# Kernel optimization log

Measured on AMD Instinct MI355X. Metric: run time of the kernel, lower is better.

## Reference

```python
import jax, jax.numpy as jnp
import numpy as np

N = 100000   # nodes
E = 800000   # edges
H = 128      # hidden_dim
HOP = 3
B = 64       # graphs


def setup_inputs() -> dict:
    key = jax.random.key(0)
    ks = jax.random.split(key, 24)
    s = 0.05
    x = jnp.round(jax.random.uniform(ks[0], (N, 1))).astype(jnp.float32)  # binary node indicator
    edge_index = jax.random.randint(ks[1], (2, E), 0, N)
    edge_attr = jax.random.normal(ks[2], (E, 1), dtype=jnp.float32)
    batch = jnp.sort(jax.random.randint(ks[3], (N,), 0, B))
    p = lambda k, sh: (s * jax.random.normal(k, sh)).astype(jnp.float32)
    return dict(
        x=x, edge_index=edge_index, edge_attr=edge_attr, batch=batch, num_graphs=B,
        l0_w=p(ks[4], (HOP, 1, H)), l0_b=p(ks[5], (HOP, H)),
        l1_w=p(ks[6], (HOP, H, H)), l1_b=p(ks[7], (HOP, H)),
        l2_w=p(ks[8], (HOP, 1, H)), l2_b=p(ks[9], (HOP, H)),
        l3_w=p(ks[10], (HOP, 1, 1)), l3_b=p(ks[11], (HOP, 1)),
        att_w=p(ks[12], (2 * H, H)), att_b=p(ks[13], (H,)),
        sp_w=p(ks[14], (H, H)), sp_b=p(ks[15], (H,)),
        ac_w=p(ks[16], (2 * H, H)), ac_b=p(ks[17], (H,)),
        last_w=p(ks[18], (2 * H, 1)), last_b=p(ks[19], (1,)),
    )


def _seg_mean(v, idx, m):
    # scatter-mean into m buckets; empty buckets -> 0 (matches PyG MeanAggregation)
    s = jax.ops.segment_sum(v, idx, num_segments=m)
    c = jax.ops.segment_sum(jnp.ones((v.shape[0], 1), v.dtype), idx, num_segments=m)
    return jnp.where(c > 0, s / jnp.maximum(c, 1.0), 0.0)


def reference(x, edge_index, edge_attr, batch, num_graphs,
              l0_w, l0_b, l1_w, l1_b, l2_w, l2_b, l3_w, l3_b,
              att_w, att_b, sp_w, sp_b, ac_w, ac_b, last_w, last_b):
    n = x.shape[0]
    row, col = edge_index[0], edge_index[1]
    hop, hid = l0_w.shape[0], l0_w.shape[2]
    u = jnp.zeros((n, hid), x.dtype)
    for i in range(hop):
        first = x @ l0_w[i] + l0_b[i]                      # [N,H]
        u_agg = _seg_mean(edge_attr * u[col], row, n)      # gather + scatter-mean
        second = u_agg @ l1_w[i] + l1_b[i]
        ee = jax.nn.relu(edge_attr @ l3_w[i] + l3_b[i])    # [E,1]
        third = _seg_mean(ee, row, n) @ l2_w[i] + l2_b[i]
        u = jax.nn.relu(first + second + third)
    # per-graph cluster embeddings (global_mean_pool ratios)
    h_c_0 = _seg_mean(u * (1 - x), batch, num_graphs) / _seg_mean(1 - x, batch, num_graphs)
    h_c_1 = _seg_mean(u * x, batch, num_graphs) / _seg_mean(x, batch, num_graphs)
    hc0, hc1 = h_c_0[batch], h_c_1[batch]                  # [N,H]
    tce = x * hc0 + (1 - x) * hc1
    h_a = jnp.concatenate([u, tce], axis=-1)               # [N,2H]
    att = h_a @ att_w + att_b
    w0 = jnp.sum(att * hc0, axis=1, keepdims=True)
    w1 = jnp.sum(att * hc1, axis=1, keepdims=True)
    w = jax.nn.softmax(jnp.concatenate([w0, w1], axis=-1), axis=-1)
    h_s = w[:, :1] * hc0 + w[:, 1:] * hc1
    q = jnp.concatenate([h_s @ sp_w + sp_b, h_a @ ac_w + ac_b], axis=-1) @ last_w + last_b
    return q
```

## Files before the change

### kernel.cpp

```cpp
#include <hip/hip_runtime.h>
#include <stdint.h>

typedef unsigned int  u32;
typedef unsigned short u16;

typedef short bf16x8 __attribute__((ext_vector_type(8)));
typedef float f32x4  __attribute__((ext_vector_type(4)));

static __device__ __forceinline__ float b2f(u16 h){
    union { u32 u; float f; } v; v.u = ((u32)h) << 16; return v.f;
}
static __device__ __forceinline__ float b2f_hi(u32 w){
    union { u32 u; float f; } v; v.u = w & 0xFFFF0000u; return v.f;
}
static __device__ __forceinline__ float b2f_lo(u32 w){
    union { u32 u; float f; } v; v.u = w << 16; return v.f;
}
static __device__ __forceinline__ u16 f2b(float f){
    union { float f; u32 u; } v; v.f = f;
    u32 r = v.u + 0x7FFFu + ((v.u >> 16) & 1u);
    return (u16)(r >> 16);
}

#define OL0W 0
#define OL0B 384
#define OL1W 768
#define OL1B 49920
#define OL2W 50304
#define OL2B 50688
#define OL3W 51072
#define OL3B 51075
#define OATTW 51078
#define OATTB 83846
#define OSPW 83974
#define OSPB 100358
#define OACW 100486
#define OACB 133254
#define OLASTW 133382
#define OLASTB 133638
#define WTOT 133639

#define PREPW_BLOCKS 192
#define ECAP 40

struct Ptrs16 { const void* p[16]; };

static __device__ __forceinline__ int detect_bf(const u32* __restrict__ xw){
    int lane = threadIdx.x & 63;
    int f = 0;
    #pragma unroll
    for (int i = 0; i < 8; ++i){
        u32 w = xw[lane * 8 + i];
        f |= ((w & 0xFFFFu) == 0x3F80u) ? 1 : 0;
    }
    return __ballot(f) != 0ull;
}

__global__ __launch_bounds__(256) void k_prep(Ptrs16 wp, const void* __restrict__ xin,
                                              float* __restrict__ wc, float* __restrict__ xc,
                                              u16* __restrict__ w1t, float* __restrict__ basev,
                                              int* __restrict__ flag,
                                              const int* __restrict__ row, const int* __restrict__ col,
                                              const void* __restrict__ ea,
                                              int* __restrict__ cnt, int2* __restrict__ ecs,
                                              int scatBase, int E, int N){
    int b = blockIdx.x, t = threadIdx.x;
    int bf = detect_bf((const u32*)xin);
    if (b >= scatBase){
        int e0 = ((b - scatBase) * 256 + t) * 4;
        if (e0 >= E) return;
        int rr[4], cc[4]; float av[4];
        if (e0 + 3 < E){
            int4 rv = *(const int4*)(row + e0);
            int4 cv = *(const int4*)(col + e0);
            rr[0]=rv.x; rr[1]=rv.y; rr[2]=rv.z; rr[3]=rv.w;
            cc[0]=cv.x; cc[1]=cv.y; cc[2]=cv.z; cc[3]=cv.w;
            if (bf){
                ushort4 ev = *(const ushort4*)((const u16*)ea + e0);
                av[0]=b2f(ev.x); av[1]=b2f(ev.y); av[2]=b2f(ev.z); av[3]=b2f(ev.w);
            } else {
                float4 ev = *(const float4*)((const float*)ea + e0);
                av[0]=ev.x; av[1]=ev.y; av[2]=ev.z; av[3]=ev.w;
            }
        } else {
            #pragma unroll
            for (int j = 0; j < 4; ++j){
                int e = e0 + j;
                rr[j] = (e < E) ? row[e] : 0;
                cc[j] = (e < E) ? col[e] : 0;
                av[j] = (e < E) ? (bf ? b2f(((const u16*)ea)[e]) : ((const float*)ea)[e]) : 0.f;
            }
        }
        int slot[4];
        #pragma unroll
        for (int j = 0; j < 4; ++j)
            slot[j] = (e0 + j < E) ? atomicAdd(&cnt[rr[j]], 1) : ECAP;
        #pragma unroll
        for (int j = 0; j < 4; ++j)
            if (e0 + j < E && slot[j] < ECAP)
                ecs[(size_t)rr[j] * ECAP + slot[j]] = make_int2(cc[j], __float_as_int(av[j]));
        return;
    }
    auto rd = [&](int seg, int off) -> float {
        return bf ? b2f(((const u16*)wp.p[seg])[off]) : ((const float*)wp.p[seg])[off];
    };
    if (b < PREPW_BLOCKS){
        int id = b * 256 + t;
        int i = id >> 14, rem = id & 16383;
        int n = rem >> 7, k = rem & 127;
        w1t[(i * 128 + n) * 128 + k] = f2b(rd(2, (i * 128 + k) * 128 + n));
        if (id < 384) basev[id] = rd(1, id) + rd(3, id) + rd(5, id);
        if (id == 0) *flag = bf;
    } else {
        int i = (b - PREPW_BLOCKS) * 256 + t;
        const int sz[16] = {384,384,49152,384,384,384,3,3,32768,128,16384,128,32768,128,256,1};
        if (i < WTOT){
            int seg = 0, off = i;
            while (off >= sz[seg]){ off -= sz[seg]; ++seg; }
            wc[i] = rd(seg, off);
        } else {
            int n = i - WTOT;
            if (n < N) xc[n] = bf ? b2f(((const u16*)xin)[n]) : ((const float*)xin)[n];
        }
    }
}

__global__ __launch_bounds__(256) void k_hop0(const int2* __restrict__ ecs, const int* __restrict__ cnt,
                                              const float* __restrict__ xc, const float* __restrict__ wc,
                                              float* __restrict__ t12,
                                              const float* __restrict__ basev, uint4* __restrict__ uOut, int N){
    int id = blockIdx.x * 256 + threadIdx.x;
    int n = id >> 4;
    if (n >= N) return;
    int sl = threadIdx.x & 15;
    float w30 = wc[OL3W + 0], w31 = wc[OL3W + 1], w32 = wc[OL3W + 2];
    float c30 = wc[OL3B + 0], c31 = wc[OL3B + 1], c32 = wc[OL3B + 2];
    int d = min(cnt[n], ECAP);
    size_t s = (size_t)n * ECAP;
    float s0 = 0.f, s1 = 0.f, s2 = 0.f;
    for (int e = sl; e < d; e += 16){
        float a = __int_as_float(ecs[s + e].y);
        s0 += fmaxf(a * w30 + c30, 0.f);
        s1 += fmaxf(a * w31 + c31, 0.f);
        s2 += fmaxf(a * w32 + c32, 0.f);
    }
    #pragma unroll
    for (int m = 1; m < 16; m <<= 1){
        s0 += __shfl_xor(s0, m);
        s1 += __shfl_xor(s1, m);
        s2 += __shfl_xor(s2, m);
    }
    float iv = d > 0 ? 1.0f / (float)d : 0.f;
    if (sl == 0){ t12[n] = s1 * iv; t12[N + n] = s2 * iv; }
    float t0 = s0 * iv;
    float xv = xc[n];
    int j = sl * 8;
    const float* l0wc = wc + OL0W;
    const float* l2wc = wc + OL2W;
    u32 w[4];
    #pragma unroll
    for (int k = 0; k < 4; ++k){
        float va = fmaxf(xv * l0wc[j + 2*k]     + t0 * l2wc[j + 2*k]     + basev[j + 2*k],     0.f);
        float vb = fmaxf(xv * l0wc[j + 2*k + 1] + t0 * l2wc[j + 2*k + 1] + basev[j + 2*k + 1], 0.f);
        w[k] = (u32)f2b(va) | ((u32)f2b(vb) << 16);
    }
    uOut[id] = make_uint4(w[0], w[1], w[2], w[3]);
}

#define ACC8(acc, g, p) \
    acc[0] += g * b2f_lo(p.x); acc[1] += g * b2f_hi(p.x); \
    acc[2] += g * b2f_lo(p.y); acc[3] += g * b2f_hi(p.y); \
    acc[4] += g * b2f_lo(p.z); acc[5] += g * b2f_hi(p.z); \
    acc[6] += g * b2f_lo(p.w); acc[7] += g * b2f_hi(p.w);

__global__ __launch_bounds__(256) void k_hop(const u16* __restrict__ uPrev, u16* __restrict__ uNext,
    const int2* __restrict__ ecs, const int* __restrict__ cnt,
    const u16* __restrict__ w1t, const float* __restrict__ basev,
    const float* __restrict__ l0wc, const float* __restrict__ l2wc,
    const float* __restrict__ xc, const float* __restrict__ t_i, int N)
{
    __shared__ __align__(16) u16 A[32][136];
    int tid = threadIdx.x;
    int lane = tid & 63, wid = tid >> 6;
    int n0 = blockIdx.x * 32;
    int cid = lane & 15, grp = lane >> 4;

    #pragma unroll
    for (int p = 0; p < 2; ++p){
        int r = wid * 8 + p * 4 + grp;
        int n = n0 + r;
        float acc[8];
        #pragma unroll
        for (int j = 0; j < 8; ++j) acc[j] = 0.f;
        if (n < N){
            int d = min(cnt[n], ECAP);
            size_t s = (size_t)n * ECAP;
            for (int e = 0; e < d; e += 8){
                int idx[8]; float g[8]; int2 m[8]; uint4 pv[8];
                idx[0] = e;
                #pragma unroll
                for (int j = 1; j < 8; ++j) idx[j] = (e + j < d) ? e + j : 0;
                #pragma unroll
                for (int j = 0; j < 8; ++j) m[j] = ecs[s + idx[j]];
                g[0] = __int_as_float(m[0].y);
                #pragma unroll
                for (int j = 1; j < 8; ++j) g[j] = (e + j < d) ? __int_as_float(m[j].y) : 0.f;
                #pragma unroll
                for (int j = 0; j < 8; ++j) pv[j] = *(const uint4*)(uPrev + (size_t)m[j].x * 128 + cid * 8);
                #pragma unroll
                for (int j = 0; j < 8; ++j){ ACC8(acc, g[j], pv[j]); }
            }
            float sc = d > 0 ? 1.0f / (float)d : 0.f;
            uint4 o;
            o.x = (u32)f2b(acc[0] * sc) | ((u32)f2b(acc[1] * sc) << 16);
            o.y = (u32)f2b(acc[2] * sc) | ((u32)f2b(acc[3] * sc) << 16);
            o.z = (u32)f2b(acc[4] * sc) | ((u32)f2b(acc[5] * sc) << 16);
            o.w = (u32)f2b(acc[6] * sc) | ((u32)f2b(acc[7] * sc) << 16);
            *(uint4*)&A[r][cid * 8] = o;
        } else {
            *(uint4*)&A[r][cid * 8] = make_uint4(0u, 0u, 0u, 0u);
        }
    }
    __syncthreads();

    bf16x8 bfr[4][2];
    #pragma unroll
    for (int kk = 0; kk < 4; ++kk)
        #pragma unroll
        for (int nt = 0; nt < 2; ++nt)
            bfr[kk][nt] = *(const bf16x8*)(w1t + (size_t)(wid * 32 + nt * 16 + cid) * 128 + kk * 32 + grp * 8);

    f32x4 acc4[2][2];
    #pragma unroll
    for (int mt = 0; mt < 2; ++mt)
        #pragma unroll
        for (int nt = 0; nt < 2; ++nt) acc4[mt][nt] = (f32x4){0.f, 0.f, 0.f, 0.f};
    #pragma unroll
    for (int kk = 0; kk < 4; ++kk){
        int kb = kk * 32 + grp * 8;
        bf16x8 af[2];
        #pragma unroll
        for (int mt = 0; mt < 2; ++mt) af[mt] = *(const bf16x8*)&A[mt * 16 + cid][kb];
        #pragma unroll
        for (int mt = 0; mt < 2; ++mt)
            #pragma unroll
            for (int nt = 0; nt < 2; ++nt)
                acc4[mt][nt] = __builtin_amdgcn_mfma_f32_16x16x32_bf16(af[mt], bfr[kk][nt], acc4[mt][nt], 0, 0, 0);
    }

    float w0c[2], w2c[2], bc[2]; int colv[2];
    #pragma unroll
    for (int nt = 0; nt < 2; ++nt){
        int col = wid * 32 + nt * 16 + cid;
        colv[nt] = col;
        w0c[nt] = l0wc[col]; w2c[nt] = l2wc[col]; bc[nt] = basev[col];
    }
    #pragma unroll
    for (int mt = 0; mt < 2; ++mt){
        #pragma unroll
        for (int rg = 0; rg < 4; ++rg){
            int n = n0 + mt * 16 + grp * 4 + rg;
            if (n < N){
                float xv = xc[n];
                float tv = t_i[n];
                #pragma unroll
                for (int nt = 0; nt < 2; ++nt){
                    float v = acc4[mt][nt][rg] + xv * w0c[nt] + tv * w2c[nt] + bc[nt];
                    uNext[(size_t)n * 128 + colv[nt]] = f2b(fmaxf(v, 0.f));
                }
            }
        }
    }
}


static __device__ __forceinline__ int lowbound(const int* b, int n, int g){
    int lo = 0, hi = n;
    while (lo < hi){ int m = (lo + hi) >> 1; if (b[m] < g) lo = m + 1; else hi = m; }
    return lo;
}

__global__ __launch_bounds__(64) void k_pool(const u32* __restrict__ u2, const float* __restrict__ xc,
                                             const int* __restrict__ batch, const float* __restrict__ wc,
                                             float* __restrict__ S0, float* __restrict__ S1,
                                             int* __restrict__ cnt1,
                                             float* __restrict__ spf, float* __restrict__ acf,
                                             float* __restrict__ biasv, int N){
    if (blockIdx.x == 2048){
        int t = threadIdx.x;
        #pragma unroll
        for (int k2 = 0; k2 < 4; ++k2){
            int rrow = t + 64 * k2;
            const float* aw = wc + OACW + rrow * 128;
            const float* lw2 = wc + OLASTW + 128;
            float s = 0.f;
            #pragma unroll 8
            for (int o = 0; o < 128; ++o) s += aw[o] * lw2[o];
            acf[rrow] = s;
        }
        #pragma unroll
        for (int k2 = 0; k2 < 2; ++k2){
            int rrow = t + 64 * k2;
            const float* sw = wc + OSPW + rrow * 128;
            const float* lw = wc + OLASTW;
            float s2 = 0.f;
            #pragma unroll 8
            for (int o = 0; o < 128; ++o) s2 += sw[o] * lw[o];
            spf[rrow] = s2;
        }
        float pb = wc[OSPB + t] * wc[OLASTW + t] + wc[OSPB + t + 64] * wc[OLASTW + t + 64]
                 + wc[OACB + t] * wc[OLASTW + 128 + t] + wc[OACB + t + 64] * wc[OLASTW + 192 + t];
        #pragma unroll
        for (int m = 1; m < 64; m <<= 1) pb += __shfl_xor(pb, m);
        if (t == 0) biasv[0] = pb + wc[OLASTB];
        return;
    }
    int g = blockIdx.x >> 5, sl = blockIdx.x & 31;
    int t = threadIdx.x;
    int st = lowbound(batch, N, g), en = lowbound(batch, N, g + 1);
    int len = en - st;
    int chunk = (len + 31) >> 5;
    int ns = st + sl * chunk;
    int ne = min(ns + chunk, en);
    float s0a = 0.f, s0b = 0.f, s1a = 0.f, s1b = 0.f; int c1 = 0;
    for (int n = ns; n < ne; ++n){
        u32 w = u2[(size_t)n * 64 + t];
        float va = b2f_lo(w), vb = b2f_hi(w);
        if (xc[n] > 0.5f){ s1a += va; s1b += vb; c1++; }
        else             { s0a += va; s0b += vb; }
    }
    atomicAdd(&S0[g * 128 + 2 * t],     s0a);
    atomicAdd(&S0[g * 128 + 2 * t + 1], s0b);
    atomicAdd(&S1[g * 128 + 2 * t],     s1a);
    atomicAdd(&S1[g * 128 + 2 * t + 1], s1b);
    if (t == 0 && c1) atomicAdd(&cnt1[g], c1);
}

__global__ __launch_bounds__(256) void k_graph(const float* __restrict__ S0, const float* __restrict__ S1,
                                               const int* __restrict__ cnt1, const int* __restrict__ batch,
                                               const float* __restrict__ wc, const float* __restrict__ spf,
                                               const float* __restrict__ acf,
                                               float* __restrict__ v0, float* __restrict__ v1,
                                               float* __restrict__ gsc, int N){
    __shared__ float h0[128], h1[128], sv0[128], sv1[128];
    int g = blockIdx.x, t = threadIdx.x;
    int st = lowbound(batch, N, g), en = lowbound(batch, N, g + 1);
    int c1 = cnt1[g], c0 = (en - st) - c1;
    if (t < 128){
        h0[t] = c0 > 0 ? S0[g * 128 + t] / (float)c0 : 0.f;
        h1[t] = c1 > 0 ? S1[g * 128 + t] / (float)c1 : 0.f;
    }
    __syncthreads();
    float a0 = 0.f, a1 = 0.f;
    for (int o = 0; o < 128; ++o){
        float w = wc[OATTW + t * 128 + o];
        a0 += w * h0[o];
        a1 += w * h1[o];
    }
    v0[g * 256 + t] = a0; v1[g * 256 + t] = a1;
    if (t >= 128){ sv0[t - 128] = a0; sv1[t - 128] = a1; }
    __syncthreads();
    if (t < 64){
        int l = t;
        float p[10];
        #pragma unroll
        for (int k = 0; k < 10; ++k) p[k] = 0.f;
        #pragma unroll
        for (int rep = 0; rep < 2; ++rep){
            int o = l + rep * 64;
            float hh0 = h0[o], hh1 = h1[o];
            float q0 = sv0[o], q1 = sv1[o];
            float ab = wc[OATTB + o];
            float sf = spf[o], af = acf[128 + o];
            p[0] += q0 * hh0; p[1] += q0 * hh1;
            p[2] += q1 * hh0; p[3] += q1 * hh1;
            p[4] += ab * hh0; p[5] += ab * hh1;
            p[6] += sf * hh0; p[7] += sf * hh1;
            p[8] += af * hh0; p[9] += af * hh1;
        }
        #pragma unroll
        for (int m = 1; m < 64; m <<= 1){
            #pragma unroll
            for (int k = 0; k < 10; ++k) p[k] += __shfl_xor(p[k], m);
        }
        if (l == 0){
            #pragma unroll
            for (int k = 0; k < 10; ++k) gsc[g * 10 + k] = p[k];
        }
    }
}

__global__ __launch_bounds__(256) void k_final(const u16* __restrict__ u, const float* __restrict__ xc,
                                               const int* __restrict__ batch,
                                               const float* __restrict__ v0, const float* __restrict__ v1,
                                               const float* __restrict__ acf, const float* __restrict__ gsc,
                                               const float* __restrict__ biasv, const int* __restrict__ flag,
                                               void* __restrict__ out, int N){
    int bf = *flag;
    int lane = threadIdx.x & 63, wid = threadIdx.x >> 6;
    int sub = lane >> 4, cid = lane & 15;
    int n = blockIdx.x * 16 + wid * 4 + sub;
    if (n >= N) return;
    int g = batch[n];
    int ch = cid * 8;
    uint4 uv = *(const uint4*)(u + (size_t)n * 128 + ch);
    const float* pv0 = v0 + g * 256 + ch;
    const float* pv1 = v1 + g * 256 + ch;
    const float* pac = acf + ch;
    float uu[8] = {b2f_lo(uv.x), b2f_hi(uv.x), b2f_lo(uv.y), b2f_hi(uv.y),
                   b2f_lo(uv.z), b2f_hi(uv.z), b2f_lo(uv.w), b2f_hi(uv.w)};
    float r0 = 0.f, r1 = 0.f, rA = 0.f;
    #pragma unroll
    for (int j = 0; j < 8; ++j){ r0 += uu[j] * pv0[j]; r1 += uu[j] * pv1[j]; rA += uu[j] * pac[j]; }
    #pragma unroll
    for (int m = 1; m < 16; m <<= 1){
        r0 += __shfl_xor(r0, m);
        r1 += __shfl_xor(r1, m);
        rA += __shfl_xor(rA, m);
    }
    if (cid == 0){
        const float* G = gsc + g * 10;
        bool xv = xc[n] > 0.5f;
        float z0 = r0 + (xv ? G[0] : G[1]) + G[4];
        float z1 = r1 + (xv ? G[2] : G[3]) + G[5];
        float mz = fmaxf(z0, z1);
        float e0 = expf(z0 - mz), e1 = expf(z1 - mz);
        float inv = 1.f / (e0 + e1);
        float q = (e0 * G[6] + e1 * G[7]) * inv + rA + (xv ? G[8] : G[9]) + biasv[0];
        if (bf) ((u16*)out)[n] = f2b(q);
        else    ((float*)out)[n] = q;
    }
}


extern "C" void kernel_launch(void* const* d_in, const int* in_sizes, int n_in,
                              void* d_out, int out_size, void* d_ws, size_t ws_size,
                              hipStream_t stream)
{
    const void* x    = d_in[0];
    const int* ei    = (const int*)d_in[1];
    const void* ea   = d_in[2];
    const int* batch = (const int*)d_in[3];
    Ptrs16 wp;
    for (int i = 0; i < 16; ++i) wp.p[i] = d_in[5 + i];

    int N = in_sizes[0];
    int E = in_sizes[2];
    const int* rowI = ei;
    const int* colI = ei + E;

    char* w = (char*)d_ws;
    size_t o = 0;
    auto alloc = [&](size_t b) -> char* {
        char* p = w + o; o = (o + b + 255) & ~(size_t)255; return p;
    };
    int*   flag   = (int*)alloc(4);
    float* basev  = (float*)alloc(3 * 128 * 4);
    float* spf    = (float*)alloc(128 * 4);
    float* acf    = (float*)alloc(256 * 4);
    float* biasv  = (float*)alloc(4);
    float* gsc    = (float*)alloc(64 * 10 * 4);
    float* v0     = (float*)alloc(64 * 256 * 4);
    float* v1     = (float*)alloc(64 * 256 * 4);
    float* wc     = (float*)alloc((size_t)WTOT * 4);
    float* xc     = (float*)alloc((size_t)N * 4);
    float* t12    = (float*)alloc((size_t)2 * N * 4);
    u16*   w1t    = (u16*)alloc((size_t)3 * 128 * 128 * 2);
    u16*   uA     = (u16*)alloc((size_t)N * 128 * 2);
    u16*   uB     = (u16*)alloc((size_t)N * 128 * 2);
    int2*  ecs    = (int2*)alloc((size_t)N * ECAP * 8);
    int*   cnt    = (int*)alloc((size_t)N * 4);
    float* S0     = (float*)alloc(64 * 128 * 4);
    float* S1     = (float*)alloc(64 * 128 * 4);
    int*   cnt1   = (int*)alloc(64 * 4);
    (void)ws_size; (void)n_in; (void)out_size;

    hipMemsetAsync(cnt, 0, (size_t)((char*)cnt1 - (char*)cnt) + 64 * 4, stream);

    int gE4 = (E / 4 + 255) / 256 + 1;
    int canonB = (WTOT + N + 255) / 256;
    int scatBase = PREPW_BLOCKS + canonB;

    k_prep<<<scatBase + gE4, 256, 0, stream>>>(wp, x, wc, xc, w1t, basev, flag,
                                               rowI, colI, ea, cnt, ecs, scatBase, E, N);
    k_hop0<<<(N * 16 + 255) / 256, 256, 0, stream>>>(ecs, cnt, xc, wc, t12, basev, (uint4*)uA, N);

    int gHop = (N + 31) / 32;
    k_hop<<<gHop, 256, 0, stream>>>(uA, uB, ecs, cnt,
                                    w1t + 1 * 16384, basev + 128, wc + OL0W + 128, wc + OL2W + 128,
                                    xc, t12, N);
    k_hop<<<gHop, 256, 0, stream>>>(uB, uA, ecs, cnt,
                                    w1t + 2 * 16384, basev + 256, wc + OL0W + 256, wc + OL2W + 256,
                                    xc, t12 + N, N);

    k_pool<<<64 * 32 + 1, 64, 0, stream>>>((const u32*)uA, xc, batch, wc, S0, S1, cnt1,
                                           spf, acf, biasv, N);
    k_graph<<<64, 256, 0, stream>>>(S0, S1, cnt1, batch, wc, spf, acf, v0, v1, gsc, N);
    k_final<<<(N + 15) / 16, 256, 0, stream>>>(uA, xc, batch, v0, v1, acf, gsc, biasv, flag, d_out, N);
}
```

Before: 316.0 us.

## Fuse graph pooling into last hop kernel and move weight folding into hop0

Removes the separate pooling kernel. The final hop kernel now accumulates per-graph sums split by the node indicator in its epilogue, reduces across lanes, and issues atomics for at most two graphs per 32-node block. Node counts are gathered with a ballot. The weight-folding work moves to an extra block of the hop0 kernel. The gather loop unroll also drops from 8 to 4 edges per iteration, which may lower register pressure but leaves fewer loads in flight. The fused path assumes each 32-node block spans at most two graphs, which relies on the batch vector being sorted and graphs being large.

```diff
diff --git a/kernel.cpp b/kernel.cpp
--- a/kernel.cpp
+++ b/kernel.cpp
@@ -127,8 +127,36 @@
 
 __global__ __launch_bounds__(256) void k_hop0(const int2* __restrict__ ecs, const int* __restrict__ cnt,
                                               const float* __restrict__ xc, const float* __restrict__ wc,
-                                              float* __restrict__ t12,
-                                              const float* __restrict__ basev, uint4* __restrict__ uOut, int N){
+                                              float* __restrict__ t12, const float* __restrict__ basev,
+                                              float* __restrict__ spf, float* __restrict__ acf,
+                                              float* __restrict__ biasv,
+                                              uint4* __restrict__ uOut, int foldBlk, int N){
+    if ((int)blockIdx.x == foldBlk){
+        int t = threadIdx.x;
+        const float* aw  = wc + OACW + t * 128;
+        const float* lw2 = wc + OLASTW + 128;
+        float s = 0.f;
+        #pragma unroll 8
+        for (int o = 0; o < 128; ++o) s += aw[o] * lw2[o];
+        acf[t] = s;
+        if (t < 128){
+            const float* sw = wc + OSPW + t * 128;
+            const float* lw = wc + OLASTW;
+            float s2 = 0.f;
+            #pragma unroll 8
+            for (int o = 0; o < 128; ++o) s2 += sw[o] * lw[o];
+            spf[t] = s2;
+        }
+        float pb = 0.f;
+        if (t < 128) pb = wc[OSPB + t] * wc[OLASTW + t] + wc[OACB + t] * wc[OLASTW + 128 + t];
+        __shared__ float red[4];
+        #pragma unroll
+        for (int m = 1; m < 64; m <<= 1) pb += __shfl_xor(pb, m);
+        if ((t & 63) == 0) red[t >> 6] = pb;
+        __syncthreads();
+        if (t == 0) biasv[0] = red[0] + red[1] + red[2] + red[3] + wc[OLASTB];
+        return;
+    }
     int id = blockIdx.x * 256 + threadIdx.x;
     int n = id >> 4;
     if (n >= N) return;
@@ -173,11 +201,14 @@
     acc[4] += g * b2f_lo(p.z); acc[5] += g * b2f_hi(p.z); \
     acc[6] += g * b2f_lo(p.w); acc[7] += g * b2f_hi(p.w);
 
+template<int POOL>
 __global__ __launch_bounds__(256) void k_hop(const u16* __restrict__ uPrev, u16* __restrict__ uNext,
     const int2* __restrict__ ecs, const int* __restrict__ cnt,
     const u16* __restrict__ w1t, const float* __restrict__ basev,
     const float* __restrict__ l0wc, const float* __restrict__ l2wc,
-    const float* __restrict__ xc, const float* __restrict__ t_i, int N)
+    const float* __restrict__ xc, const float* __restrict__ t_i,
+    const int* __restrict__ batch, float* __restrict__ S0, float* __restrict__ S1,
+    int* __restrict__ cnt1, int N)
 {
     __shared__ __align__(16) u16 A[32][136];
     int tid = threadIdx.x;
@@ -195,20 +226,21 @@
         if (n < N){
             int d = min(cnt[n], ECAP);
             size_t s = (size_t)n * ECAP;
-            for (int e = 0; e < d; e += 8){
-                int idx[8]; float g[8]; int2 m[8]; uint4 pv[8];
-                idx[0] = e;
-                #pragma unroll
-                for (int j = 1; j < 8; ++j) idx[j] = (e + j < d) ? e + j : 0;
-                #pragma unroll
-                for (int j = 0; j < 8; ++j) m[j] = ecs[s + idx[j]];
-                g[0] = __int_as_float(m[0].y);
-                #pragma unroll
-                for (int j = 1; j < 8; ++j) g[j] = (e + j < d) ? __int_as_float(m[j].y) : 0.f;
-                #pragma unroll
-                for (int j = 0; j < 8; ++j) pv[j] = *(const uint4*)(uPrev + (size_t)m[j].x * 128 + cid * 8);
-                #pragma unroll
-                for (int j = 0; j < 8; ++j){ ACC8(acc, g[j], pv[j]); }
+            for (int e = 0; e < d; e += 4){
+                int i1 = (e + 1 < d) ? e + 1 : 0;
+                int i2 = (e + 2 < d) ? e + 2 : 0;
+                int i3 = (e + 3 < d) ? e + 3 : 0;
+                int2 m0 = ecs[s + e], m1 = ecs[s + i1], m2 = ecs[s + i2], m3 = ecs[s + i3];
+                float g0 = __int_as_float(m0.y);
+                float g1 = (e + 1 < d) ? __int_as_float(m1.y) : 0.f;
+                float g2 = (e + 2 < d) ? __int_as_float(m2.y) : 0.f;
+                float g3 = (e + 3 < d) ? __int_as_float(m3.y) : 0.f;
+                uint4 p0 = *(const uint4*)(uPrev + (size_t)m0.x * 128 + cid * 8);
+                uint4 p1 = *(const uint4*)(uPrev + (size_t)m1.x * 128 + cid * 8);
+                uint4 p2 = *(const uint4*)(uPrev + (size_t)m2.x * 128 + cid * 8);
+                uint4 p3 = *(const uint4*)(uPrev + (size_t)m3.x * 128 + cid * 8);
+                ACC8(acc, g0, p0); ACC8(acc, g1, p1);
+                ACC8(acc, g2, p2); ACC8(acc, g3, p3);
             }
             float sc = d > 0 ? 1.0f / (float)d : 0.f;
             uint4 o;
@@ -255,6 +287,14 @@
         colv[nt] = col;
         w0c[nt] = l0wc[col]; w2c[nt] = l2wc[col]; bc[nt] = basev[col];
     }
+    int gLo = 0, gHi = 0;
+    float accP[8];
+    if (POOL){
+        gLo = batch[n0];
+        gHi = batch[min(n0 + 31, N - 1)];
+        #pragma unroll
+        for (int j = 0; j < 8; ++j) accP[j] = 0.f;
+    }
     #pragma unroll
     for (int mt = 0; mt < 2; ++mt){
         #pragma unroll
@@ -263,11 +303,48 @@
             if (n < N){
                 float xv = xc[n];
                 float tv = t_i[n];
+                int sel = 0;
+                if (POOL){
+                    sel = ((batch[n] != gLo) ? 2 : 0) + ((xv > 0.5f) ? 1 : 0);
+                }
                 #pragma unroll
                 for (int nt = 0; nt < 2; ++nt){
-                    float v = acc4[mt][nt][rg] + xv * w0c[nt] + tv * w2c[nt] + bc[nt];
-                    uNext[(size_t)n * 128 + colv[nt]] = f2b(fmaxf(v, 0.f));
+                    float v = fmaxf(acc4[mt][nt][rg] + xv * w0c[nt] + tv * w2c[nt] + bc[nt], 0.f);
+                    uNext[(size_t)n * 128 + colv[nt]] = f2b(v);
+                    if (POOL) accP[nt * 4 + sel] += v;
                 }
+            }
+        }
+    }
+    if (POOL){
+        #pragma unroll
+        for (int j = 0; j < 8; ++j){
+            accP[j] += __shfl_xor(accP[j], 16);
+            accP[j] += __shfl_xor(accP[j], 32);
+        }
+        if (grp == 0){
+            #pragma unroll
+            for (int nt = 0; nt < 2; ++nt){
+                atomicAdd(&S0[gLo * 128 + colv[nt]], accP[nt * 4 + 0]);
+                atomicAdd(&S1[gLo * 128 + colv[nt]], accP[nt * 4 + 1]);
+                if (gHi != gLo){
+                    atomicAdd(&S0[gHi * 128 + colv[nt]], accP[nt * 4 + 2]);
+                    atomicAdd(&S1[gHi * 128 + colv[nt]], accP[nt * 4 + 3]);
+                }
+            }
+        }
+        if (wid == 0){
+            int n = n0 + lane;
+            int ok = (lane < 32 && n < N) ? 1 : 0;
+            int is1 = ok && (xc[n] > 0.5f);
+            int hi  = ok && (batch[n] != gLo);
+            unsigned long long mLo = __ballot(is1 && !hi);
+            unsigned long long mHi = __ballot(is1 && hi);
+            if (lane == 0){
+                int c = __popcll(mLo);
+                if (c) atomicAdd(&cnt1[gLo], c);
+                c = __popcll(mHi);
+                if (c && gHi != gLo) atomicAdd(&cnt1[gHi], c);
             }
         }
     }
@@ -278,62 +355,6 @@
     int lo = 0, hi = n;
     while (lo < hi){ int m = (lo + hi) >> 1; if (b[m] < g) lo = m + 1; else hi = m; }
     return lo;
-}
-
-__global__ __launch_bounds__(64) void k_pool(const u32* __restrict__ u2, const float* __restrict__ xc,
-                                             const int* __restrict__ batch, const float* __restrict__ wc,
-                                             float* __restrict__ S0, float* __restrict__ S1,
-                                             int* __restrict__ cnt1,
-                                             float* __restrict__ spf, float* __restrict__ acf,
-                                             float* __restrict__ biasv, int N){
-    if (blockIdx.x == 2048){
-        int t = threadIdx.x;
-        #pragma unroll
-        for (int k2 = 0; k2 < 4; ++k2){
-            int rrow = t + 64 * k2;
-            const float* aw = wc + OACW + rrow * 128;
-            const float* lw2 = wc + OLASTW + 128;
-            float s = 0.f;
-            #pragma unroll 8
-            for (int o = 0; o < 128; ++o) s += aw[o] * lw2[o];
-            acf[rrow] = s;
-        }
-        #pragma unroll
-        for (int k2 = 0; k2 < 2; ++k2){
-            int rrow = t + 64 * k2;
-            const float* sw = wc + OSPW + rrow * 128;
-            const float* lw = wc + OLASTW;
-            float s2 = 0.f;
-            #pragma unroll 8
-            for (int o = 0; o < 128; ++o) s2 += sw[o] * lw[o];
-            spf[rrow] = s2;
-        }
-        float pb = wc[OSPB + t] * wc[OLASTW + t] + wc[OSPB + t + 64] * wc[OLASTW + t + 64]
-                 + wc[OACB + t] * wc[OLASTW + 128 + t] + wc[OACB + t + 64] * wc[OLASTW + 192 + t];
-        #pragma unroll
-        for (int m = 1; m < 64; m <<= 1) pb += __shfl_xor(pb, m);
-        if (t == 0) biasv[0] = pb + wc[OLASTB];
-        return;
-    }
-    int g = blockIdx.x >> 5, sl = blockIdx.x & 31;
-    int t = threadIdx.x;
-    int st = lowbound(batch, N, g), en = lowbound(batch, N, g + 1);
-    int len = en - st;
-    int chunk = (len + 31) >> 5;
-    int ns = st + sl * chunk;
-    int ne = min(ns + chunk, en);
-    float s0a = 0.f, s0b = 0.f, s1a = 0.f, s1b = 0.f; int c1 = 0;
-    for (int n = ns; n < ne; ++n){
-        u32 w = u2[(size_t)n * 64 + t];
-        float va = b2f_lo(w), vb = b2f_hi(w);
-        if (xc[n] > 0.5f){ s1a += va; s1b += vb; c1++; }
-        else             { s0a += va; s0b += vb; }
-    }
-    atomicAdd(&S0[g * 128 + 2 * t],     s0a);
-    atomicAdd(&S0[g * 128 + 2 * t + 1], s0b);
-    atomicAdd(&S1[g * 128 + 2 * t],     s1a);
-    atomicAdd(&S1[g * 128 + 2 * t + 1], s1b);
-    if (t == 0 && c1) atomicAdd(&cnt1[g], c1);
 }
 
 __global__ __launch_bounds__(256) void k_graph(const float* __restrict__ S0, const float* __restrict__ S1,
@@ -483,18 +504,18 @@
 
     k_prep<<<scatBase + gE4, 256, 0, stream>>>(wp, x, wc, xc, w1t, basev, flag,
                                                rowI, colI, ea, cnt, ecs, scatBase, E, N);
-    k_hop0<<<(N * 16 + 255) / 256, 256, 0, stream>>>(ecs, cnt, xc, wc, t12, basev, (uint4*)uA, N);
+    int gHop0 = (N * 16 + 255) / 256;
+    k_hop0<<<gHop0 + 1, 256, 0, stream>>>(ecs, cnt, xc, wc, t12, basev, spf, acf, biasv,
+                                          (uint4*)uA, gHop0, N);
 
     int gHop = (N + 31) / 32;
-    k_hop<<<gHop, 256, 0, stream>>>(uA, uB, ecs, cnt,
-                                    w1t + 1 * 16384, basev + 128, wc + OL0W + 128, wc + OL2W + 128,
-                                    xc, t12, N);
-    k_hop<<<gHop, 256, 0, stream>>>(uB, uA, ecs, cnt,
-                                    w1t + 2 * 16384, basev + 256, wc + OL0W + 256, wc + OL2W + 256,
-                                    xc, t12 + N, N);
-
-    k_pool<<<64 * 32 + 1, 64, 0, stream>>>((const u32*)uA, xc, batch, wc, S0, S1, cnt1,
-                                           spf, acf, biasv, N);
+    k_hop<0><<<gHop, 256, 0, stream>>>(uA, uB, ecs, cnt,
+                                       w1t + 1 * 16384, basev + 128, wc + OL0W + 128, wc + OL2W + 128,
+                                       xc, t12, batch, S0, S1, cnt1, N);
+    k_hop<1><<<gHop, 256, 0, stream>>>(uB, uA, ecs, cnt,
+                                       w1t + 2 * 16384, basev + 256, wc + OL0W + 256, wc + OL2W + 256,
+                                       xc, t12 + N, batch, S0, S1, cnt1, N);
+
     k_graph<<<64, 256, 0, stream>>>(S0, S1, cnt1, batch, wc, spf, acf, v0, v1, gsc, N);
     k_final<<<(N + 15) / 16, 256, 0, stream>>>(uA, xc, batch, v0, v1, acf, gsc, biasv, flag, d_out, N);
 }
```

Result: faster. 303.2 us (-4.0%).
